# Performance work log

Measured on AMD Instinct MI355X. Metric: run time of the kernel, lower is better.

Reference implementation:

```python
import jax, jax.numpy as jnp
import numpy as np

D_MODEL = 1024
N_HEADS = 16
HEAD = D_MODEL // N_HEADS  # 64


def setup_inputs() -> dict:
    key = jax.random.key(0)
    ks = jax.random.split(key, 6)
    B, T = 2, 2048
    x = jax.random.normal(ks[0], (B, T, D_MODEL), dtype=jnp.float32)
    s_in = 1.0 / np.sqrt(HEAD)
    # per-head projections: Linear(head_size -> d_model), no bias. Stored as [H, head, d_model].
    Wq = jax.random.normal(ks[1], (N_HEADS, HEAD, D_MODEL), dtype=jnp.float32) * s_in
    Wk = jax.random.normal(ks[2], (N_HEADS, HEAD, D_MODEL), dtype=jnp.float32) * s_in
    Wv = jax.random.normal(ks[3], (N_HEADS, HEAD, D_MODEL), dtype=jnp.float32) * s_in
    # output projection: Linear(H*d_model -> d_model) with bias
    Wo = jax.random.normal(ks[4], (N_HEADS * D_MODEL, D_MODEL), dtype=jnp.float32) / np.sqrt(N_HEADS * D_MODEL)
    bo = jax.random.normal(ks[5], (D_MODEL,), dtype=jnp.float32) * 0.01
    return {"x": x, "Wq": Wq, "Wk": Wk, "Wv": Wv, "Wo": Wo, "bo": bo}


def reference(x, Wq, Wk, Wv, Wo, bo):
    B, T, _ = x.shape
    # split into per-head slices: [B, H, T, head]
    xh = x.reshape(B, T, N_HEADS, HEAD).transpose(0, 2, 1, 3)
    q = jnp.einsum("bhtd,hdm->bhtm", xh, Wq)  # [B,H,T,d_model]
    k = jnp.einsum("bhtd,hdm->bhtm", xh, Wk)
    v = jnp.einsum("bhtd,hdm->bhtm", xh, Wv)
    # scale uses D = head input dim (= HEAD), per the original code
    scores = jnp.einsum("bhtm,bhsm->bhts", q, k) / jnp.sqrt(jnp.asarray(HEAD, x.dtype))
    weights = jax.nn.softmax(scores, axis=-1)
    vb = jnp.einsum("bhts,bhsm->bhtm", weights, v)  # [B,H,T,d_model]
    cat = vb.transpose(0, 2, 1, 3).reshape(B, T, N_HEADS * D_MODEL)
    return cat @ Wo + bo
```

## Files before the change

### kernel.cpp

```cpp
#include <hip/hip_runtime.h>
#include <math.h>

typedef unsigned u32;
typedef unsigned short u16;
typedef __attribute__((ext_vector_type(8))) __bf16 bf16x8;
typedef __attribute__((ext_vector_type(4))) float f32x4;

#define DEVI __device__ __forceinline__

DEVI u16 f2bf(float f) {
    u32 u = __builtin_bit_cast(u32, f);
    u += 0x7fffu + ((u >> 16) & 1u);
    return (u16)(u >> 16);
}

DEVI u32 packbf(float a, float b) {
    u32 ua = __builtin_bit_cast(u32, a) + 0x8000u;
    u32 ub = __builtin_bit_cast(u32, b) + 0x8000u;
    return (ua >> 16) | (ub & 0xffff0000u);
}

DEVI bf16x8 ldsf(const u16* p) { return *(const bf16x8*)p; }

DEVI f32x4 mfma16(bf16x8 a, bf16x8 b, f32x4 c) {
    return __builtin_amdgcn_mfma_f32_16x16x32_bf16(a, b, c, 0, 0, 0);
}

#if __has_builtin(__builtin_amdgcn_exp2f)
DEVI float fexp2(float x) { return __builtin_amdgcn_exp2f(x); }
#else
DEVI float fexp2(float x) { return exp2f(x); }
#endif

__global__ __launch_bounds__(256) void k_pw(const float* __restrict__ x,
                                            const float* __restrict__ Wq, const float* __restrict__ Wk,
                                            const float* __restrict__ Wv, const float* __restrict__ Wo,
                                            u16* __restrict__ xswz, u16* __restrict__ xt2,
                                            u16* __restrict__ mtg, u16* __restrict__ W2) {
    __shared__ __align__(16) char SM[18432];
    const int tid = threadIdx.x;
    const int id = blockIdx.x;
    const int rr = tid >> 2, c16 = (tid & 3) * 16;

    if (id < 272) {
        u16* LA = (u16*)SM;
        u16* LB = (u16*)(SM + 9216);
        const int w = tid >> 6, lane = tid & 63, g = lane >> 4, ln = lane & 15;
        f32x4 acc[4] = {};
        float4 pa[4], pb[4];

        if (id >= 256) {
            const int h = id - 256;
            {
                const float4* sa = (const float4*)(Wk + (h * 64 + rr) * 1024 + c16);
                const float4* sb = (const float4*)(Wq + (h * 64 + rr) * 1024 + c16);
#pragma unroll
                for (int j = 0; j < 4; j++) { pa[j] = sa[j]; pb[j] = sb[j]; }
            }
            for (int kb = 0; kb < 16; kb++) {
                __syncthreads();
                {
                    union { uint4 q[2]; u16 s[16]; } ua, ub;
#pragma unroll
                    for (int j = 0; j < 4; j++) {
                        ua.s[j*4+0]=f2bf(pa[j].x); ua.s[j*4+1]=f2bf(pa[j].y); ua.s[j*4+2]=f2bf(pa[j].z); ua.s[j*4+3]=f2bf(pa[j].w);
                        ub.s[j*4+0]=f2bf(pb[j].x); ub.s[j*4+1]=f2bf(pb[j].y); ub.s[j*4+2]=f2bf(pb[j].z); ub.s[j*4+3]=f2bf(pb[j].w);
                    }
                    *(uint4*)(LA + rr * 72 + c16) = ua.q[0]; *(uint4*)(LA + rr * 72 + c16 + 8) = ua.q[1];
                    *(uint4*)(LB + rr * 72 + c16) = ub.q[0]; *(uint4*)(LB + rr * 72 + c16 + 8) = ub.q[1];
                }
                __syncthreads();
                if (kb < 15) {
                    const float4* sa = (const float4*)(Wk + (h * 64 + rr) * 1024 + (kb + 1) * 64 + c16);
                    const float4* sb = (const float4*)(Wq + (h * 64 + rr) * 1024 + (kb + 1) * 64 + c16);
#pragma unroll
                    for (int j = 0; j < 4; j++) { pa[j] = sa[j]; pb[j] = sb[j]; }
                }
#pragma unroll
                for (int ks = 0; ks < 2; ks++) {
                    bf16x8 bb = ldsf(LB + (w * 16 + ln) * 72 + ks * 32 + g * 8);
#pragma unroll
                    for (int mt = 0; mt < 4; mt++) {
                        bf16x8 a = ldsf(LA + (mt * 16 + ln) * 72 + ks * 32 + g * 8);
                        acc[mt] = mfma16(a, bb, acc[mt]);
                    }
                }
            }
#pragma unroll
            for (int mt = 0; mt < 4; mt++)
#pragma unroll
                for (int r = 0; r < 4; r++)
                    mtg[h * 4096 + (mt * 16 + g * 4 + r) * 64 + w * 16 + ln] =
                        f2bf(acc[mt][r] * 0.18033688011112f);
        } else {
            const int h = id >> 4, n0 = (id & 15) * 64;
            {
                const float4* sa = (const float4*)(Wo + (h * 1024 + rr) * 1024 + n0 + c16);
                const float4* sb = (const float4*)(Wv + (h * 64 + rr) * 1024 + c16);
#pragma unroll
                for (int j = 0; j < 4; j++) { pa[j] = sa[j]; pb[j] = sb[j]; }
            }
            for (int kb = 0; kb < 16; kb++) {
                __syncthreads();
                {
                    union { uint4 q[2]; u16 s[16]; } ub;
#pragma unroll
                    for (int j = 0; j < 4; j++) {
                        ub.s[j*4+0]=f2bf(pb[j].x); ub.s[j*4+1]=f2bf(pb[j].y); ub.s[j*4+2]=f2bf(pb[j].z); ub.s[j*4+3]=f2bf(pb[j].w);
                    }
                    *(uint4*)(LB + rr * 72 + c16) = ub.q[0]; *(uint4*)(LB + rr * 72 + c16 + 8) = ub.q[1];
#pragma unroll
                    for (int j = 0; j < 4; j++) {
                        LA[(c16 + j * 4 + 0) * 72 + rr] = f2bf(pa[j].x);
                        LA[(c16 + j * 4 + 1) * 72 + rr] = f2bf(pa[j].y);
                        LA[(c16 + j * 4 + 2) * 72 + rr] = f2bf(pa[j].z);
                        LA[(c16 + j * 4 + 3) * 72 + rr] = f2bf(pa[j].w);
                    }
                }
                __syncthreads();
                if (kb < 15) {
                    const float4* sa = (const float4*)(Wo + (h * 1024 + (kb + 1) * 64 + rr) * 1024 + n0 + c16);
                    const float4* sb = (const float4*)(Wv + (h * 64 + rr) * 1024 + (kb + 1) * 64 + c16);
#pragma unroll
                    for (int j = 0; j < 4; j++) { pa[j] = sa[j]; pb[j] = sb[j]; }
                }
#pragma unroll
                for (int ks = 0; ks < 2; ks++) {
                    bf16x8 bb = ldsf(LB + (w * 16 + ln) * 72 + ks * 32 + g * 8);
#pragma unroll
                    for (int mt = 0; mt < 4; mt++) {
                        bf16x8 a = ldsf(LA + (mt * 16 + ln) * 72 + ks * 32 + g * 8);
                        acc[mt] = mfma16(a, bb, acc[mt]);
                    }
                }
            }
            int d = w * 16 + ln;
#pragma unroll
            for (int mt = 0; mt < 4; mt++)
#pragma unroll
                for (int r = 0; r < 4; r++) {
                    int n = n0 + mt * 16 + g * 4 + r;
                    W2[h * 65536 + n * 64 + (((d >> 3) ^ (n & 7)) << 3) + (d & 7)] = f2bf(acc[mt][r]);
                }
        }
    } else {
        const int pid = id - 272;
        const int kt = pid & 31, h = (pid >> 5) & 15, b = pid >> 9, bh = b * 16 + h;
        float* T = (float*)SM;
        int t = kt * 64 + rr;
        const float4* gx = (const float4*)(x + (b * 2048 + t) * 1024 + h * 64 + c16);
        float4 f[4];
#pragma unroll
        for (int j = 0; j < 4; j++) f[j] = gx[j];
#pragma unroll
        for (int j = 0; j < 4; j++) {
            T[rr * 65 + c16 + j * 4 + 0] = f[j].x; T[rr * 65 + c16 + j * 4 + 1] = f[j].y;
            T[rr * 65 + c16 + j * 4 + 2] = f[j].z; T[rr * 65 + c16 + j * 4 + 3] = f[j].w;
        }
        {
            union { uint4 q[2]; u16 s[16]; } u;
#pragma unroll
            for (int j = 0; j < 4; j++) {
                u.s[j * 4 + 0] = f2bf(f[j].x); u.s[j * 4 + 1] = f2bf(f[j].y);
                u.s[j * 4 + 2] = f2bf(f[j].z); u.s[j * 4 + 3] = f2bf(f[j].w);
            }
            u16* dst = xswz + (bh * 2048 + t) * 64;
            int c0 = (tid & 3) * 2, sw = rr & 7;
            *(uint4*)(dst + ((c0 ^ sw) << 3))       = u.q[0];
            *(uint4*)(dst + (((c0 + 1) ^ sw) << 3)) = u.q[1];
        }
        __syncthreads();
        int dd = tid >> 2, t4 = (tid & 3) * 16;
        union { uint2 d2[4]; u16 s[16]; } ou;
#pragma unroll
        for (int j = 0; j < 16; j++) ou.s[j] = f2bf(T[(t4 + j) * 65 + dd]);
        u16* dst = xt2 + bh * 131072 + kt * 4096 + dd * 64;
        const int nt0 = t4 >> 4;
        const int cb = (nt0 >> 1) * 4;
        const int off = (nt0 & 1) * 4;
        const int sw = dd & 7;
#pragma unroll
        for (int g4 = 0; g4 < 4; g4++) {
            int c = cb + g4;
            *(uint2*)(dst + ((c ^ sw) << 3) + off) = ou.d2[g4];
        }
    }
}

__global__ __launch_bounds__(256, 2) void k_attn(const u16* __restrict__ xswz, const u16* __restrict__ xt2,
                                                 const u16* __restrict__ mtg, u16* __restrict__ U2) {
    __shared__ __align__(16) u16 smem[16384];
    u16* KB = smem;
    u16* VB = smem + 8192;

    const int tid = threadIdx.x;
    const int w = tid >> 6, lane = tid & 63, g = lane >> 4, ln = lane & 15, ln7 = lane & 7;
    const int nid = (blockIdx.x & 7) * 64 + (blockIdx.x >> 3);
    const int qt = nid & 15, h = (nid >> 4) & 15, b = nid >> 8, bh = b * 16 + h;
    const u16* xs = xswz + bh * 131072;
    const u16* xv = xt2 + bh * 131072;

    bf16x8 qf[2][2];
    {
        u16* LM  = smem;
        u16* LXQ = smem + 4608;
        {
            int r4 = tid >> 2, c4 = (tid & 3) * 2;
            const uint4* gm = (const uint4*)(mtg + h * 4096 + r4 * 64);
            uint4 m0 = gm[c4], m1 = gm[c4 + 1];
            *(uint4*)(LM + r4 * 72 + c4 * 8)     = m0;
            *(uint4*)(LM + r4 * 72 + c4 * 8 + 8) = m1;
            int r2 = tid >> 1, c2 = (tid & 1) * 4;
            const uint4* gx = (const uint4*)(xs + (qt * 128 + r2) * 64);
            uint4 x0 = gx[c2], x1 = gx[c2 + 1], x2 = gx[c2 + 2], x3 = gx[c2 + 3];
            *(uint4*)(LXQ + r2 * 72 + c2 * 8)      = x0;
            *(uint4*)(LXQ + r2 * 72 + c2 * 8 + 8)  = x1;
            *(uint4*)(LXQ + r2 * 72 + c2 * 8 + 16) = x2;
            *(uint4*)(LXQ + r2 * 72 + c2 * 8 + 24) = x3;
        }
        __syncthreads();
        f32x4 acc[2][4] = {};
#pragma unroll
        for (int qh = 0; qh < 2; qh++) {
            int row = qh * 64 + w * 16 + ln;
#pragma unroll
            for (int ks = 0; ks < 2; ks++) {
                bf16x8 a = ldsf(LXQ + row * 72 + (((ks * 4 + g) ^ ln7) << 3));
#pragma unroll
                for (int nt = 0; nt < 4; nt++) {
                    bf16x8 bb = ldsf(LM + (nt * 16 + ln) * 72 + ks * 32 + g * 8);
                    acc[qh][nt] = mfma16(a, bb, acc[qh][nt]);
                }
            }
        }
        __syncthreads();
#pragma unroll
        for (int qh = 0; qh < 2; qh++) {
            u16* QLw = smem + qh * 4608 + w * 1152;
#pragma unroll
            for (int nt = 0; nt < 4; nt++)
#pragma unroll
                for (int r = 0; r < 4; r++)
                    QLw[(g * 4 + r) * 72 + nt * 16 + ln] = f2bf(acc[qh][nt][r]);
        }
        asm volatile("s_waitcnt lgkmcnt(0)" ::: "memory");
#pragma unroll
        for (int qh = 0; qh < 2; qh++) {
            u16* QLw = smem + qh * 4608 + w * 1152;
            qf[qh][0] = ldsf(QLw + ln * 72 + g * 8);
            qf[qh][1] = ldsf(QLw + ln * 72 + 32 + g * 8);
        }
        __syncthreads();
    }

    {
        const uint4* gk = (const uint4*)xs;
        const uint4* gv = (const uint4*)xv;
        uint4 k0 = gk[tid], k1 = gk[tid + 256], v0 = gv[tid], v1 = gv[tid + 256];
        uint4* lk = (uint4*)KB;
        uint4* lv = (uint4*)VB;
        lk[tid] = k0; lk[tid + 256] = k1; lv[tid] = v0; lv[tid + 256] = v1;
    }
    __syncthreads();

    float lrow[2] = {0.f, 0.f};
    f32x4 o[2][4] = {};

#pragma unroll 2
    for (int kt = 0; kt < 32; ++kt) {
        const int cur = (kt & 1) << 12;
        const u16* KL = KB + cur;
        const u16* VL = VB + cur;

        uint4 kr0, kr1, vr0, vr1;
        if (kt + 1 < 32) {
            const uint4* gk = (const uint4*)(xs + (kt + 1) * 4096);
            const uint4* gv = (const uint4*)(xv + (kt + 1) * 4096);
            kr0 = gk[tid]; kr1 = gk[tid + 256]; vr0 = gv[tid]; vr1 = gv[tid + 256];
        }

        f32x4 s[2][4] = {};
        __builtin_amdgcn_s_setprio(1);
#pragma unroll
        for (int ks = 0; ks < 2; ks++) {
#pragma unroll
            for (int nt = 0; nt < 4; nt++) {
                bf16x8 a = ldsf(KL + (nt * 16 + ln) * 64 + (((ks * 4 + g) ^ ln7) << 3));
                s[0][nt] = mfma16(a, qf[0][ks], s[0][nt]);
                s[1][nt] = mfma16(a, qf[1][ks], s[1][nt]);
            }
        }
        __builtin_amdgcn_s_setprio(0);

        u32 pk[2][4][2];
#pragma unroll
        for (int qh = 0; qh < 2; qh++) {
            float ts = 0.f;
#pragma unroll
            for (int nt = 0; nt < 4; nt++) {
                float p0 = fexp2(s[qh][nt][0]), p1 = fexp2(s[qh][nt][1]);
                float p2 = fexp2(s[qh][nt][2]), p3 = fexp2(s[qh][nt][3]);
                pk[qh][nt][0] = packbf(p0, p1);
                pk[qh][nt][1] = packbf(p2, p3);
                ts += (p0 + p1) + (p2 + p3);
            }
            lrow[qh] += ts;
        }

        __builtin_amdgcn_s_setprio(1);
#pragma unroll
        for (int ks = 0; ks < 2; ks++) {
            union { u32 u[4]; bf16x8 v; } pf[2];
#pragma unroll
            for (int qh = 0; qh < 2; qh++) {
                pf[qh].u[0] = pk[qh][2 * ks][0];
                pf[qh].u[1] = pk[qh][2 * ks][1];
                pf[qh].u[2] = pk[qh][2 * ks + 1][0];
                pf[qh].u[3] = pk[qh][2 * ks + 1][1];
            }
#pragma unroll
            for (int dt = 0; dt < 4; dt++) {
                bf16x8 a = ldsf(VL + (dt * 16 + ln) * 64 + (((ks * 4 + g) ^ ln7) << 3));
                o[0][dt] = mfma16(a, pf[0].v, o[0][dt]);
                o[1][dt] = mfma16(a, pf[1].v, o[1][dt]);
            }
        }
        __builtin_amdgcn_s_setprio(0);

        if (kt + 1 < 32) {
            const int nxt = cur ^ 4096;
            uint4* lk = (uint4*)(KB + nxt);
            uint4* lv = (uint4*)(VB + nxt);
            lk[tid] = kr0; lk[tid + 256] = kr1; lv[tid] = vr0; lv[tid + 256] = vr1;
        }
        __syncthreads();
    }

#pragma unroll
    for (int qh = 0; qh < 2; qh++) {
        lrow[qh] += __shfl_xor(lrow[qh], 16, 64);
        lrow[qh] += __shfl_xor(lrow[qh], 32, 64);
        float inv = 1.0f / lrow[qh];
        int t = b * 2048 + qt * 128 + qh * 64 + w * 16 + ln;
#pragma unroll
        for (int dt = 0; dt < 4; dt++) {
            ushort4 vv;
            vv.x = f2bf(o[qh][dt][0] * inv); vv.y = f2bf(o[qh][dt][1] * inv);
            vv.z = f2bf(o[qh][dt][2] * inv); vv.w = f2bf(o[qh][dt][3] * inv);
            int c = dt * 2 + (g >> 1);
            int pos = c ^ (t & 7);
            *(ushort4*)(U2 + h * 262144 + t * 64 + pos * 8 + (g & 1) * 4) = vv;
        }
    }
}

__global__ __launch_bounds__(512) void k_out(const u16* __restrict__ U2, const u16* __restrict__ W2,
                                             const float* __restrict__ bo, float* __restrict__ out) {
    __shared__ __align__(16) u16 SMu[32768];
    const int tid = threadIdx.x;
    const int w = tid >> 6, lane = tid & 63, g = lane >> 4, ln = lane & 15;
    const int nid = (blockIdx.x & 7) * 32 + (blockIdx.x >> 3);
    const int n0 = (nid & 7) * 128, r0 = (nid >> 3) * 128;
    const int wr = (w >> 2) * 64, wc = (w & 3) * 32;
    f32x4 acc[4][2] = {};
    uint4 ar[2], br[2];

    {
        const uint4* ga = (const uint4*)(U2 + r0 * 64);
        const uint4* gb = (const uint4*)(W2 + n0 * 64);
        ar[0] = ga[tid]; ar[1] = ga[tid + 512];
        br[0] = gb[tid]; br[1] = gb[tid + 512];
        ((uint4*)SMu)[tid] = ar[0]; ((uint4*)SMu)[tid + 512] = ar[1];
        ((uint4*)(SMu + 16384))[tid] = br[0]; ((uint4*)(SMu + 16384))[tid + 512] = br[1];
    }
    asm volatile("s_waitcnt lgkmcnt(0)" ::: "memory");
    __builtin_amdgcn_s_barrier();
    __builtin_amdgcn_sched_barrier(0);

    for (int kb = 0; kb < 16; kb++) {
        const int cu = (kb & 1) << 13;
        if (kb + 1 < 16) {
            const uint4* ga = (const uint4*)(U2 + (kb + 1) * 262144 + r0 * 64);
            const uint4* gb = (const uint4*)(W2 + (kb + 1) * 65536 + n0 * 64);
            ar[0] = ga[tid]; ar[1] = ga[tid + 512];
            br[0] = gb[tid]; br[1] = gb[tid + 512];
        }
        const u16* AL = SMu + cu;
        const u16* BL = SMu + 16384 + cu;
#pragma unroll
        for (int ks = 0; ks < 2; ks++) {
            bf16x8 af[4], bfr[2];
#pragma unroll
            for (int mt = 0; mt < 4; mt++) {
                int rr = wr + mt * 16 + ln;
                af[mt] = ldsf(AL + rr * 64 + (((ks * 4 + g) ^ (rr & 7)) << 3));
            }
#pragma unroll
            for (int nt = 0; nt < 2; nt++) {
                int rr = wc + nt * 16 + ln;
                bfr[nt] = ldsf(BL + rr * 64 + (((ks * 4 + g) ^ (rr & 7)) << 3));
            }
#pragma unroll
            for (int mt = 0; mt < 4; mt++)
#pragma unroll
                for (int nt = 0; nt < 2; nt++)
                    acc[mt][nt] = mfma16(af[mt], bfr[nt], acc[mt][nt]);
        }
        if (kb + 1 < 16) {
            const int nx = cu ^ 8192;
            uint4* la = (uint4*)(SMu + nx);
            uint4* lb = (uint4*)(SMu + 16384 + nx);
            la[tid] = ar[0]; la[tid + 512] = ar[1];
            lb[tid] = br[0]; lb[tid + 512] = br[1];
        }
        asm volatile("s_waitcnt lgkmcnt(0)" ::: "memory");
        __builtin_amdgcn_s_barrier();
        __builtin_amdgcn_sched_barrier(0);
    }

    float* Wp = (float*)SMu + w * 576;
    const int coff = (lane & 7) * 4;
    const float4 b4 = *(const float4*)(bo + n0 + wc + coff);
#pragma unroll
    for (int mt = 0; mt < 4; mt++) {
#pragma unroll
        for (int nt = 0; nt < 2; nt++)
#pragma unroll
            for (int r = 0; r < 4; r++)
                Wp[(g * 4 + r) * 36 + nt * 16 + ln] = acc[mt][nt][r];
        asm volatile("s_waitcnt lgkmcnt(0)" ::: "memory");
#pragma unroll
        for (int i = 0; i < 2; i++) {
            int row = (lane >> 3) + 8 * i;
            float4 v = *(const float4*)(Wp + row * 36 + coff);
            v.x += b4.x; v.y += b4.y; v.z += b4.z; v.w += b4.w;
            *(float4*)(out + (r0 + wr + mt * 16 + row) * 1024 + n0 + wc + coff) = v;
        }
    }
}

extern "C" void kernel_launch(void* const* d_in, const int* in_sizes, int n_in,
                              void* d_out, int out_size, void* d_ws, size_t ws_size,
                              hipStream_t stream) {
    const float* x  = (const float*)d_in[0];
    const float* Wq = (const float*)d_in[1];
    const float* Wk = (const float*)d_in[2];
    const float* Wv = (const float*)d_in[3];
    const float* Wo = (const float*)d_in[4];
    const float* bo = (const float*)d_in[5];
    float* out = (float*)d_out;

    char* ws = (char*)d_ws;
    u16* xswz = (u16*)(ws);
    u16* mtg  = (u16*)(ws + 8388608);
    u16* xt2  = (u16*)(ws + 8519680);
    u16* W2   = (u16*)(ws + 16908288);
    u16* U2   = (u16*)(ws + 19005440);

    k_pw<<<1296, 256, 0, stream>>>(x, Wq, Wk, Wv, Wo, xswz, xt2, mtg, W2);
    k_attn<<<512, 256, 0, stream>>>(xswz, xt2, mtg, U2);
    k_out<<<256, 512, 0, stream>>>(U2, W2, bo, out);
}
```

Measured before the change: 203.4 us.

## Double-buffer weight prep GEMM and load V fragments directly into registers

In the weight-precompute kernel, the single LDS stage becomes two LDS buffers with register prefetch two tiles ahead, using one lighter barrier per half-step instead of two __syncthreads per tile. In the attention kernel, V tiles no longer pass through shared memory. Each lane loads its swizzled MFMA fragments straight from global memory into double-buffered registers, which cuts LDS traffic and leaves only K in LDS. The cost is higher register pressure (16 bf16x8 V fragments on a launch_bounds(256,2) kernel) and uncoalesced 16-byte global loads for V.

```diff
diff --git a/kernel.cpp b/kernel.cpp
--- a/kernel.cpp
+++ b/kernel.cpp
@@ -37,54 +37,68 @@
                                             const float* __restrict__ Wv, const float* __restrict__ Wo,
                                             u16* __restrict__ xswz, u16* __restrict__ xt2,
                                             u16* __restrict__ mtg, u16* __restrict__ W2) {
-    __shared__ __align__(16) char SM[18432];
+    __shared__ __align__(16) char SM[36864];
     const int tid = threadIdx.x;
     const int id = blockIdx.x;
     const int rr = tid >> 2, c16 = (tid & 3) * 16;
 
     if (id < 272) {
-        u16* LA = (u16*)SM;
-        u16* LB = (u16*)(SM + 9216);
+        u16* LA0 = (u16*)SM;
+        u16* LB0 = (u16*)(SM + 9216);
+        u16* LA1 = (u16*)(SM + 18432);
+        u16* LB1 = (u16*)(SM + 27648);
         const int w = tid >> 6, lane = tid & 63, g = lane >> 4, ln = lane & 15;
         f32x4 acc[4] = {};
-        float4 pa[4], pb[4];
+        float4 pa0[4], pb0[4], pa1[4], pb1[4];
+
+        auto mm = [&](const u16* LAp, const u16* LBp) {
+#pragma unroll
+            for (int ks = 0; ks < 2; ks++) {
+                bf16x8 bb = ldsf(LBp + (w * 16 + ln) * 72 + ks * 32 + g * 8);
+#pragma unroll
+                for (int mt = 0; mt < 4; mt++) {
+                    bf16x8 a = ldsf(LAp + (mt * 16 + ln) * 72 + ks * 32 + g * 8);
+                    acc[mt] = mfma16(a, bb, acc[mt]);
+                }
+            }
+        };
+        auto bar = [&]() {
+            asm volatile("s_waitcnt lgkmcnt(0)" ::: "memory");
+            __builtin_amdgcn_s_barrier();
+            __builtin_amdgcn_sched_barrier(0);
+        };
 
         if (id >= 256) {
             const int h = id - 256;
-            {
-                const float4* sa = (const float4*)(Wk + (h * 64 + rr) * 1024 + c16);
-                const float4* sb = (const float4*)(Wq + (h * 64 + rr) * 1024 + c16);
+            auto loadT = [&](int t, float4* pa, float4* pb) {
+                const float4* sa = (const float4*)(Wk + (h * 64 + rr) * 1024 + t * 64 + c16);
+                const float4* sb = (const float4*)(Wq + (h * 64 + rr) * 1024 + t * 64 + c16);
 #pragma unroll
                 for (int j = 0; j < 4; j++) { pa[j] = sa[j]; pb[j] = sb[j]; }
-            }
-            for (int kb = 0; kb < 16; kb++) {
-                __syncthreads();
-                {
-                    union { uint4 q[2]; u16 s[16]; } ua, ub;
-#pragma unroll
-                    for (int j = 0; j < 4; j++) {
-                        ua.s[j*4+0]=f2bf(pa[j].x); ua.s[j*4+1]=f2bf(pa[j].y); ua.s[j*4+2]=f2bf(pa[j].z); ua.s[j*4+3]=f2bf(pa[j].w);
-                        ub.s[j*4+0]=f2bf(pb[j].x); ub.s[j*4+1]=f2bf(pb[j].y); ub.s[j*4+2]=f2bf(pb[j].z); ub.s[j*4+3]=f2bf(pb[j].w);
-                    }
-                    *(uint4*)(LA + rr * 72 + c16) = ua.q[0]; *(uint4*)(LA + rr * 72 + c16 + 8) = ua.q[1];
-                    *(uint4*)(LB + rr * 72 + c16) = ub.q[0]; *(uint4*)(LB + rr * 72 + c16 + 8) = ub.q[1];
-                }
-                __syncthreads();
-                if (kb < 15) {
-                    const float4* sa = (const float4*)(Wk + (h * 64 + rr) * 1024 + (kb + 1) * 64 + c16);
-                    const float4* sb = (const float4*)(Wq + (h * 64 + rr) * 1024 + (kb + 1) * 64 + c16);
-#pragma unroll
-                    for (int j = 0; j < 4; j++) { pa[j] = sa[j]; pb[j] = sb[j]; }
-                }
-#pragma unroll
-                for (int ks = 0; ks < 2; ks++) {
-                    bf16x8 bb = ldsf(LB + (w * 16 + ln) * 72 + ks * 32 + g * 8);
-#pragma unroll
-                    for (int mt = 0; mt < 4; mt++) {
-                        bf16x8 a = ldsf(LA + (mt * 16 + ln) * 72 + ks * 32 + g * 8);
-                        acc[mt] = mfma16(a, bb, acc[mt]);
-                    }
-                }
+            };
+            auto cvtW = [&](u16* LAp, u16* LBp, float4* pa, float4* pb) {
+                union { uint4 q[2]; u16 s[16]; } ua, ub;
+#pragma unroll
+                for (int j = 0; j < 4; j++) {
+                    ua.s[j*4+0]=f2bf(pa[j].x); ua.s[j*4+1]=f2bf(pa[j].y); ua.s[j*4+2]=f2bf(pa[j].z); ua.s[j*4+3]=f2bf(pa[j].w);
+                    ub.s[j*4+0]=f2bf(pb[j].x); ub.s[j*4+1]=f2bf(pb[j].y); ub.s[j*4+2]=f2bf(pb[j].z); ub.s[j*4+3]=f2bf(pb[j].w);
+                }
+                *(uint4*)(LAp + rr * 72 + c16) = ua.q[0]; *(uint4*)(LAp + rr * 72 + c16 + 8) = ua.q[1];
+                *(uint4*)(LBp + rr * 72 + c16) = ub.q[0]; *(uint4*)(LBp + rr * 72 + c16 + 8) = ub.q[1];
+            };
+            loadT(0, pa0, pb0);
+            cvtW(LA0, LB0, pa0, pb0);
+            loadT(1, pa1, pb1);
+            bar();
+            for (int kb = 0; kb < 16; kb += 2) {
+                if (kb + 2 < 16) loadT(kb + 2, pa0, pb0);
+                mm(LA0, LB0);
+                cvtW(LA1, LB1, pa1, pb1);
+                bar();
+                if (kb + 3 < 16) loadT(kb + 3, pa1, pb1);
+                mm(LA1, LB1);
+                if (kb + 2 < 16) cvtW(LA0, LB0, pa0, pb0);
+                bar();
             }
 #pragma unroll
             for (int mt = 0; mt < 4; mt++)
@@ -94,45 +108,40 @@
                         f2bf(acc[mt][r] * 0.18033688011112f);
         } else {
             const int h = id >> 4, n0 = (id & 15) * 64;
-            {
-                const float4* sa = (const float4*)(Wo + (h * 1024 + rr) * 1024 + n0 + c16);
-                const float4* sb = (const float4*)(Wv + (h * 64 + rr) * 1024 + c16);
+            auto loadT = [&](int t, float4* pa, float4* pb) {
+                const float4* sa = (const float4*)(Wo + (h * 1024 + t * 64 + rr) * 1024 + n0 + c16);
+                const float4* sb = (const float4*)(Wv + (h * 64 + rr) * 1024 + t * 64 + c16);
 #pragma unroll
                 for (int j = 0; j < 4; j++) { pa[j] = sa[j]; pb[j] = sb[j]; }
-            }
-            for (int kb = 0; kb < 16; kb++) {
-                __syncthreads();
-                {
-                    union { uint4 q[2]; u16 s[16]; } ub;
-#pragma unroll
-                    for (int j = 0; j < 4; j++) {
-                        ub.s[j*4+0]=f2bf(pb[j].x); ub.s[j*4+1]=f2bf(pb[j].y); ub.s[j*4+2]=f2bf(pb[j].z); ub.s[j*4+3]=f2bf(pb[j].w);
-                    }
-                    *(uint4*)(LB + rr * 72 + c16) = ub.q[0]; *(uint4*)(LB + rr * 72 + c16 + 8) = ub.q[1];
-#pragma unroll
-                    for (int j = 0; j < 4; j++) {
-                        LA[(c16 + j * 4 + 0) * 72 + rr] = f2bf(pa[j].x);
-                        LA[(c16 + j * 4 + 1) * 72 + rr] = f2bf(pa[j].y);
-                        LA[(c16 + j * 4 + 2) * 72 + rr] = f2bf(pa[j].z);
-                        LA[(c16 + j * 4 + 3) * 72 + rr] = f2bf(pa[j].w);
-                    }
-                }
-                __syncthreads();
-                if (kb < 15) {
-                    const float4* sa = (const float4*)(Wo + (h * 1024 + (kb + 1) * 64 + rr) * 1024 + n0 + c16);
-                    const float4* sb = (const float4*)(Wv + (h * 64 + rr) * 1024 + (kb + 1) * 64 + c16);
-#pragma unroll
-                    for (int j = 0; j < 4; j++) { pa[j] = sa[j]; pb[j] = sb[j]; }
-                }
-#pragma unroll
-                for (int ks = 0; ks < 2; ks++) {
-                    bf16x8 bb = ldsf(LB + (w * 16 + ln) * 72 + ks * 32 + g * 8);
-#pragma unroll
-                    for (int mt = 0; mt < 4; mt++) {
-                        bf16x8 a = ldsf(LA + (mt * 16 + ln) * 72 + ks * 32 + g * 8);
-                        acc[mt] = mfma16(a, bb, acc[mt]);
-                    }
-                }
+            };
+            auto cvtW = [&](u16* LAp, u16* LBp, float4* pa, float4* pb) {
+                union { uint4 q[2]; u16 s[16]; } ub;
+#pragma unroll
+                for (int j = 0; j < 4; j++) {
+                    ub.s[j*4+0]=f2bf(pb[j].x); ub.s[j*4+1]=f2bf(pb[j].y); ub.s[j*4+2]=f2bf(pb[j].z); ub.s[j*4+3]=f2bf(pb[j].w);
+                }
+                *(uint4*)(LBp + rr * 72 + c16) = ub.q[0]; *(uint4*)(LBp + rr * 72 + c16 + 8) = ub.q[1];
+#pragma unroll
+                for (int j = 0; j < 4; j++) {
+                    LAp[(c16 + j * 4 + 0) * 72 + rr] = f2bf(pa[j].x);
+                    LAp[(c16 + j * 4 + 1) * 72 + rr] = f2bf(pa[j].y);
+                    LAp[(c16 + j * 4 + 2) * 72 + rr] = f2bf(pa[j].z);
+                    LAp[(c16 + j * 4 + 3) * 72 + rr] = f2bf(pa[j].w);
+                }
+            };
+            loadT(0, pa0, pb0);
+            cvtW(LA0, LB0, pa0, pb0);
+            loadT(1, pa1, pb1);
+            bar();
+            for (int kb = 0; kb < 16; kb += 2) {
+                if (kb + 2 < 16) loadT(kb + 2, pa0, pb0);
+                mm(LA0, LB0);
+                cvtW(LA1, LB1, pa1, pb1);
+                bar();
+                if (kb + 3 < 16) loadT(kb + 3, pa1, pb1);
+                mm(LA1, LB1);
+                if (kb + 2 < 16) cvtW(LA0, LB0, pa0, pb0);
+                bar();
             }
             int d = w * 16 + ln;
 #pragma unroll
@@ -191,7 +200,6 @@
                                                  const u16* __restrict__ mtg, u16* __restrict__ U2) {
     __shared__ __align__(16) u16 smem[16384];
     u16* KB = smem;
-    u16* VB = smem + 8192;
 
     const int tid = threadIdx.x;
     const int w = tid >> 6, lane = tid & 63, g = lane >> 4, ln = lane & 15, ln7 = lane & 7;
@@ -255,28 +263,36 @@
 
     {
         const uint4* gk = (const uint4*)xs;
-        const uint4* gv = (const uint4*)xv;
-        uint4 k0 = gk[tid], k1 = gk[tid + 256], v0 = gv[tid], v1 = gv[tid + 256];
+        uint4 k0 = gk[tid], k1 = gk[tid + 256];
         uint4* lk = (uint4*)KB;
-        uint4* lv = (uint4*)VB;
-        lk[tid] = k0; lk[tid + 256] = k1; lv[tid] = v0; lv[tid + 256] = v1;
-    }
-    __syncthreads();
+        lk[tid] = k0; lk[tid + 256] = k1;
+    }
+    bf16x8 vfA[2][4], vfB[2][4];
+#pragma unroll
+    for (int ks = 0; ks < 2; ks++)
+#pragma unroll
+        for (int dt = 0; dt < 4; dt++)
+            vfA[ks][dt] = *(const bf16x8*)(xv + (dt * 16 + ln) * 64 + (((ks * 4 + g) ^ ln7) << 3));
+    asm volatile("s_waitcnt lgkmcnt(0)" ::: "memory");
+    __builtin_amdgcn_s_barrier();
+    __builtin_amdgcn_sched_barrier(0);
 
     float lrow[2] = {0.f, 0.f};
     f32x4 o[2][4] = {};
 
-#pragma unroll 2
-    for (int kt = 0; kt < 32; ++kt) {
+    auto step = [&](int kt, bf16x8 (&vcur)[2][4], bf16x8 (&vnxt)[2][4]) {
         const int cur = (kt & 1) << 12;
         const u16* KL = KB + cur;
-        const u16* VL = VB + cur;
-
-        uint4 kr0, kr1, vr0, vr1;
+        uint4 kr0, kr1;
         if (kt + 1 < 32) {
             const uint4* gk = (const uint4*)(xs + (kt + 1) * 4096);
-            const uint4* gv = (const uint4*)(xv + (kt + 1) * 4096);
-            kr0 = gk[tid]; kr1 = gk[tid + 256]; vr0 = gv[tid]; vr1 = gv[tid + 256];
+            kr0 = gk[tid]; kr1 = gk[tid + 256];
+            const u16* gv = xv + (kt + 1) * 4096;
+#pragma unroll
+            for (int ks = 0; ks < 2; ks++)
+#pragma unroll
+                for (int dt = 0; dt < 4; dt++)
+                    vnxt[ks][dt] = *(const bf16x8*)(gv + (dt * 16 + ln) * 64 + (((ks * 4 + g) ^ ln7) << 3));
         }
 
         f32x4 s[2][4] = {};
@@ -320,9 +336,8 @@
             }
 #pragma unroll
             for (int dt = 0; dt < 4; dt++) {
-                bf16x8 a = ldsf(VL + (dt * 16 + ln) * 64 + (((ks * 4 + g) ^ ln7) << 3));
-                o[0][dt] = mfma16(a, pf[0].v, o[0][dt]);
-                o[1][dt] = mfma16(a, pf[1].v, o[1][dt]);
+                o[0][dt] = mfma16(vcur[ks][dt], pf[0].v, o[0][dt]);
+                o[1][dt] = mfma16(vcur[ks][dt], pf[1].v, o[1][dt]);
             }
         }
         __builtin_amdgcn_s_setprio(0);
@@ -330,10 +345,16 @@
         if (kt + 1 < 32) {
             const int nxt = cur ^ 4096;
             uint4* lk = (uint4*)(KB + nxt);
-            uint4* lv = (uint4*)(VB + nxt);
-            lk[tid] = kr0; lk[tid + 256] = kr1; lv[tid] = vr0; lv[tid + 256] = vr1;
-        }
-        __syncthreads();
+            lk[tid] = kr0; lk[tid + 256] = kr1;
+        }
+        asm volatile("s_waitcnt lgkmcnt(0)" ::: "memory");
+        __builtin_amdgcn_s_barrier();
+        __builtin_amdgcn_sched_barrier(0);
+    };
+
+    for (int kt = 0; kt < 32; kt += 2) {
+        step(kt, vfA, vfB);
+        step(kt + 1, vfB, vfA);
     }
 
 #pragma unroll
```

Result: slower. 207.8 us (+2.2%).
